# Optimization experiments

Hardware: AMD Instinct MI355X
Metric: run time of the kernel (lower is better)

The kernel has to match this reference:

```python
import jax, jax.numpy as jnp
import numpy as np

DIM = 512
H = 8
HD = DIM // H  # head_dim = 64


def setup_inputs() -> dict:
    key = jax.random.key(0)
    k1, k2, k3 = jax.random.split(key, 3)
    B, N = 16, 4096
    x = jax.random.normal(k1, (B, DIM, N), jnp.float32)
    # qkv_proj: Conv1d(dim, H*(1+2*HD), kernel=1) == linear over channels
    Wqkv = jax.random.normal(k2, (H * (1 + 2 * HD), DIM), jnp.float32) * 0.02
    bqkv = jnp.zeros((H * (1 + 2 * HD),), jnp.float32)
    # proj: Conv1d(dim, dim, kernel=1)
    Wp = jax.random.normal(k3, (DIM, DIM), jnp.float32) * 0.02
    bp = jnp.zeros((DIM,), jnp.float32)
    return {"x": x, "Wqkv": Wqkv, "bqkv": bqkv, "Wp": Wp, "bp": bp}


def reference(x, Wqkv, bqkv, Wp, bp):
    B, C, N = x.shape
    # 1x1 conv projection -> [B, H*(1+2*HD), N]
    qkv = jnp.einsum('oc,bcn->bon', Wqkv, x) + bqkv[None, :, None]
    qkv = qkv.reshape(B, H, 1 + 2 * HD, N)
    q = qkv[:, :, 0:1, :]          # [B,H,1,N]
    k = qkv[:, :, 1:1 + HD, :]     # [B,H,HD,N]
    v = qkv[:, :, 1 + HD:, :]      # [B,H,HD,N]
    scores = jax.nn.softmax(q, axis=-1)              # softmax over N
    ctx = jnp.sum(k * scores, axis=-1, keepdims=True)  # [B,H,HD,1]
    out = jax.nn.relu(v) * ctx                         # [B,H,HD,N]
    # permute/split/cat in torch == [B,H,HD,N] -> [B,N,H*HD] -> [B,C,N]
    out = out.transpose(0, 3, 1, 2).reshape(B, N, H * HD)
    out = out.transpose(0, 2, 1)                       # [B,C,N]
    out = jnp.einsum('oc,bcn->bon', Wp, out) + bp[None, :, None]
    return out
```

## Files before the change

kernel.cpp:

```cpp
#include <hip/hip_runtime.h>

#define NB 16
#define NC 512
#define NN 4096
#define NH 8

typedef __attribute__((ext_vector_type(8))) __bf16 bf16x8;
typedef __attribute__((ext_vector_type(4))) float f32x4;

__device__ __forceinline__ unsigned short f2bf(float f) {
    union { float f; unsigned u; } x; x.f = f;
    unsigned r = x.u + 0x7FFF + ((x.u >> 16) & 1);
    return (unsigned short)(r >> 16);
}
__device__ __forceinline__ float bits2f(unsigned u) {
    union { unsigned u; float f; } x; x.u = u; return x.f;
}

__global__ void pack_kernel(const float* __restrict__ Wqkv, const float* __restrict__ bqkv,
                            const float* __restrict__ Wp,
                            unsigned short* __restrict__ Wv_bf, unsigned short* __restrict__ Wp_bf,
                            float* __restrict__ bv) {
    int t = blockIdx.x * 256 + threadIdx.x;
    int j = t >> 9, c = t & 511;
    int h = j >> 6, d = j & 63;
    Wv_bf[t] = f2bf(Wqkv[((size_t)h * 129 + 65 + d) * 512 + c]);
    Wp_bf[t] = f2bf(Wp[t]);
    if (t < 512) bv[t] = bqkv[(t >> 6) * 129 + 65 + (t & 63)];
}

__global__ void transpose_q_kernel(const float* __restrict__ x, const float* __restrict__ Wqkv,
                                   unsigned short* __restrict__ xT, float* __restrict__ qP) {
    __shared__ unsigned short tile[64][66];
    __shared__ float Ws[8][64];
    __shared__ float qw[4][8][64];
    int b = blockIdx.z, c0 = blockIdx.y * 64, n0 = blockIdx.x * 64;
    int t = threadIdx.x;
    for (int i = t; i < 512; i += 256)
        Ws[i >> 6][i & 63] = Wqkv[(size_t)(i >> 6) * (129 * 512) + c0 + (i & 63)];
    __syncthreads();
    int r = t >> 4, cc = (t & 15) * 4;
    const float* xp = x + ((size_t)b * NC + c0) * NN + n0;
    float accq[8][4];
#pragma unroll
    for (int h = 0; h < 8; h++)
#pragma unroll
        for (int j = 0; j < 4; j++) accq[h][j] = 0.f;
#pragma unroll
    for (int p = 0; p < 4; p++) {
        int row = r + p * 16;
        float4 v = *(const float4*)(xp + (size_t)row * NN + cc);
        tile[row][cc + 0] = f2bf(v.x);
        tile[row][cc + 1] = f2bf(v.y);
        tile[row][cc + 2] = f2bf(v.z);
        tile[row][cc + 3] = f2bf(v.w);
#pragma unroll
        for (int h = 0; h < 8; h++) {
            float w = Ws[h][row];
            accq[h][0] += w * v.x;
            accq[h][1] += w * v.y;
            accq[h][2] += w * v.z;
            accq[h][3] += w * v.w;
        }
    }
    __syncthreads();
    {
        int j = t >> 2, cg = (t & 3) * 16;
        alignas(16) unsigned short tmp[16];
#pragma unroll
        for (int i = 0; i < 16; i++) tmp[i] = tile[cg + i][j];
        unsigned short* dst = xT + ((size_t)b * NN + n0 + j) * NC + c0 + cg;
        *(uint4*)(dst) = *(const uint4*)(tmp);
        *(uint4*)(dst + 8) = *(const uint4*)(tmp + 8);
    }
    int lane = t & 63, w = t >> 6;
#pragma unroll
    for (int h = 0; h < 8; h++)
#pragma unroll
        for (int j = 0; j < 4; j++) {
            float a = accq[h][j];
            a += __shfl_xor(a, 16);
            a += __shfl_xor(a, 32);
            accq[h][j] = a;
        }
    if (lane < 16) {
#pragma unroll
        for (int h = 0; h < 8; h++)
#pragma unroll
            for (int j = 0; j < 4; j++) qw[w][h][lane * 4 + j] = accq[h][j];
    }
    __syncthreads();
    for (int i = t; i < 512; i += 256) {
        int h = i >> 6, n = i & 63;
        float s = qw[0][h][n] + qw[1][h][n] + qw[2][h][n] + qw[3][h][n];
        qP[(((size_t)blockIdx.y * NB + b) * 8 + h) * NN + n0 + n] = s;
    }
}

__global__ void softmax_kernel(const float* __restrict__ qP, float* __restrict__ sT) {
    int bh = blockIdx.x;
    int b = bh >> 3, h = bh & 7;
    int t = threadIdx.x;
    __shared__ float red[8];
    const float* qp = qP + (size_t)bh * NN;
    const size_t cstr = (size_t)NB * 8 * NN;
    float v[16];
    float mx = -1e30f;
#pragma unroll
    for (int i = 0; i < 16; i++) {
        int n = t + i * 256;
        float s = 0.f;
#pragma unroll
        for (int cb = 0; cb < 8; cb++) s += qp[cb * cstr + n];
        v[i] = s; mx = fmaxf(mx, s);
    }
#pragma unroll
    for (int o = 32; o; o >>= 1) mx = fmaxf(mx, __shfl_xor(mx, o));
    if ((t & 63) == 0) red[t >> 6] = mx;
    __syncthreads();
    mx = fmaxf(fmaxf(red[0], red[1]), fmaxf(red[2], red[3]));
    float s = 0.f;
#pragma unroll
    for (int i = 0; i < 16; i++) { v[i] = __expf(v[i] - mx); s += v[i]; }
#pragma unroll
    for (int o = 32; o; o >>= 1) s += __shfl_xor(s, o);
    __syncthreads();
    if ((t & 63) == 0) red[4 + (t >> 6)] = s;
    __syncthreads();
    float inv = 1.f / (red[4] + red[5] + red[6] + red[7]);
#pragma unroll
    for (int i = 0; i < 16; i++) {
        int n = t + i * 256;
        sT[((size_t)b * NN + n) * 8 + h] = v[i] * inv;
    }
}

__global__ void xbar_kernel(const unsigned short* __restrict__ xT, const float* __restrict__ sT,
                            float* __restrict__ xbarP) {
    int b = blockIdx.y, sl = blockIdx.x;
    int t = threadIdx.x;
    int g = __builtin_amdgcn_readfirstlane(t >> 6);
    int lane = t & 63;
    int c8 = lane * 8;
    int nbase = sl * 256 + g * 64;
    float acc[8][8];
#pragma unroll
    for (int h = 0; h < 8; h++)
#pragma unroll
        for (int c = 0; c < 8; c++) acc[h][c] = 0.f;
    const unsigned short* xp = xT + ((size_t)b * NN + nbase) * NC + c8;
    const float* sp = sT + ((size_t)b * NN + nbase) * 8;
    for (int i = 0; i < 64; i++) {
        uint4 xv = *(const uint4*)(xp + (size_t)i * NC);
        float xf[8];
        xf[0] = bits2f(xv.x << 16); xf[1] = bits2f(xv.x & 0xFFFF0000u);
        xf[2] = bits2f(xv.y << 16); xf[3] = bits2f(xv.y & 0xFFFF0000u);
        xf[4] = bits2f(xv.z << 16); xf[5] = bits2f(xv.z & 0xFFFF0000u);
        xf[6] = bits2f(xv.w << 16); xf[7] = bits2f(xv.w & 0xFFFF0000u);
#pragma unroll
        for (int h = 0; h < 8; h++) {
            float s = sp[i * 8 + h];
#pragma unroll
            for (int c = 0; c < 8; c++) acc[h][c] += s * xf[c];
        }
    }
#pragma unroll
    for (int h = 0; h < 8; h++) {
        float* dst = xbarP + (((size_t)(sl * 4 + g) * NB + b) * 8 + h) * NC + c8;
        f32x4 lo = {acc[h][0], acc[h][1], acc[h][2], acc[h][3]};
        f32x4 hi = {acc[h][4], acc[h][5], acc[h][6], acc[h][7]};
        *(f32x4*)(dst) = lo;
        *(f32x4*)(dst + 4) = hi;
    }
}

__global__ void ctx_kernel(const float* __restrict__ xbarP, const float* __restrict__ Wqkv,
                           const float* __restrict__ bqkv, float* __restrict__ ctx) {
    int bh = blockIdx.x; int b = bh >> 3, h = bh & 7;
    int t = threadIdx.x;
    __shared__ float xb[512];
    for (int i = t; i < 512; i += 256) {
        float s = 0.f;
        for (int sl = 0; sl < 64; sl++) s += xbarP[(((size_t)sl * NB + b) * 8 + h) * NC + i];
        xb[i] = s;
    }
    __syncthreads();
    int d = t >> 2, sub = t & 3;
    const float* wk = Wqkv + ((size_t)h * 129 + 1 + d) * 512;
    float acc = 0.f;
    for (int i = sub * 4; i < 512; i += 16) {
        float4 w = *(const float4*)(wk + i);
        acc += w.x * xb[i] + w.y * xb[i + 1] + w.z * xb[i + 2] + w.w * xb[i + 3];
    }
    acc += __shfl_xor(acc, 1);
    acc += __shfl_xor(acc, 2);
    if (sub == 0) ctx[(size_t)b * NC + h * 64 + d] = acc + bqkv[h * 129 + 1 + d];
}

template <int MODE>
__global__ __launch_bounds__(512) void gemm_kernel(
    const unsigned short* __restrict__ A,
    const unsigned short* __restrict__ Bmat,
    const float* __restrict__ bias,
    const float* __restrict__ ctx,
    unsigned short* __restrict__ mT,
    float* __restrict__ outp)
{
    __shared__ alignas(16) unsigned short As[256 * 32];
    __shared__ alignas(16) unsigned short Bs[128 * 32];
    int b = blockIdx.z;
    int m0 = blockIdx.y * 256, n0 = blockIdx.x * 128;
    int t = threadIdx.x;
    int lane = t & 63;
    int wid = t >> 6;
    int wm = wid >> 1, wn = wid & 1;

    const unsigned short* Bb = Bmat + ((size_t)b * NN + n0) * NC;

    f32x4 acc[4][4];
#pragma unroll
    for (int i = 0; i < 4; i++)
#pragma unroll
        for (int j = 0; j < 4; j++) { f32x4 z = {0.f, 0.f, 0.f, 0.f}; acc[i][j] = z; }

    for (int kk = 0; kk < 512; kk += 32) {
        {
            int u = t, row = u >> 2, kg = u & 3;
            uint4 va = *(const uint4*)(A + (size_t)(m0 + row) * 512 + kk + kg * 8);
            *(uint4*)(As + (size_t)u * 8) = va;
            u = t + 512; row = u >> 2; kg = u & 3;
            uint4 vb = *(const uint4*)(A + (size_t)(m0 + row) * 512 + kk + kg * 8);
            *(uint4*)(As + (size_t)u * 8) = vb;
            u = t; row = u >> 2; kg = u & 3;
            uint4 vc = *(const uint4*)(Bb + (size_t)row * 512 + kk + kg * 8);
            *(uint4*)(Bs + (size_t)u * 8) = vc;
        }
        __syncthreads();
        bf16x8 af[4], bfr[4];
        int koff = (lane >> 4) * 8;
        int arow = wm * 64 + (lane & 15);
        int brow = wn * 64 + (lane & 15);
#pragma unroll
        for (int i = 0; i < 4; i++) af[i]  = *(const bf16x8*)(As + (size_t)(arow + i * 16) * 32 + koff);
#pragma unroll
        for (int j = 0; j < 4; j++) bfr[j] = *(const bf16x8*)(Bs + (size_t)(brow + j * 16) * 32 + koff);
#pragma unroll
        for (int i = 0; i < 4; i++)
#pragma unroll
            for (int j = 0; j < 4; j++)
                acc[i][j] = __builtin_amdgcn_mfma_f32_16x16x32_bf16(af[i], bfr[j], acc[i][j], 0, 0, 0);
        __syncthreads();
    }

    int g = lane >> 4, col = lane & 15;
#pragma unroll
    for (int i = 0; i < 4; i++) {
        int j0 = m0 + wm * 64 + i * 16 + g * 4;
        if (MODE == 0) {
            float4 bv4 = *(const float4*)(bias + j0);
            float4 cx4 = *(const float4*)(ctx + (size_t)b * NC + j0);
#pragma unroll
            for (int j = 0; j < 4; j++) {
                int n = n0 + wn * 64 + j * 16 + col;
                f32x4 a = acc[i][j];
                unsigned short h0 = f2bf(fmaxf(a[0] + bv4.x, 0.f) * cx4.x);
                unsigned short h1 = f2bf(fmaxf(a[1] + bv4.y, 0.f) * cx4.y);
                unsigned short h2 = f2bf(fmaxf(a[2] + bv4.z, 0.f) * cx4.z);
                unsigned short h3 = f2bf(fmaxf(a[3] + bv4.w, 0.f) * cx4.w);
                uint2 pk;
                pk.x = (unsigned)h0 | ((unsigned)h1 << 16);
                pk.y = (unsigned)h2 | ((unsigned)h3 << 16);
                *(uint2*)(mT + ((size_t)b * NN + n) * NC + j0) = pk;
            }
        } else {
            float4 bp4 = *(const float4*)(bias + j0);
#pragma unroll
            for (int j = 0; j < 4; j++) {
                int n = n0 + wn * 64 + j * 16 + col;
                f32x4 a = acc[i][j];
                float* op = outp + (size_t)b * NC * NN + (size_t)j0 * NN + n;
                op[0]              = a[0] + bp4.x;
                op[NN]             = a[1] + bp4.y;
                op[2 * (size_t)NN] = a[2] + bp4.z;
                op[3 * (size_t)NN] = a[3] + bp4.w;
            }
        }
    }
}

extern "C" void kernel_launch(void* const* d_in, const int* in_sizes, int n_in,
                              void* d_out, int out_size, void* d_ws, size_t ws_size,
                              hipStream_t stream) {
    const float* x    = (const float*)d_in[0];
    const float* Wqkv = (const float*)d_in[1];
    const float* bqkv = (const float*)d_in[2];
    const float* Wp   = (const float*)d_in[3];
    const float* bp   = (const float*)d_in[4];
    float* outp = (float*)d_out;

    char* ws = (char*)d_ws;
    unsigned short* mT = (unsigned short*)ws;
    float* sT    = (float*)(ws + 2097152);
    float* qP    = (float*)(ws + 4194304);
    float* xbarP = (float*)(ws + 20971520);
    float* ctx   = (float*)(ws + 67108864);
    unsigned short* Wv_bf = (unsigned short*)(ws + 67108864 + 32768);
    unsigned short* Wp_bf = (unsigned short*)(ws + 67108864 + 32768 + 524288);
    float* bv    = (float*)(ws + 67108864 + 32768 + 1048576);
    unsigned short* xT = (unsigned short*)d_out;

    pack_kernel<<<dim3(1024), 256, 0, stream>>>(Wqkv, bqkv, Wp, Wv_bf, Wp_bf, bv);
    transpose_q_kernel<<<dim3(64, 8, 16), 256, 0, stream>>>(x, Wqkv, xT, qP);
    softmax_kernel<<<dim3(128), 256, 0, stream>>>(qP, sT);
    xbar_kernel<<<dim3(16, 16), 256, 0, stream>>>(xT, sT, xbarP);
    ctx_kernel<<<dim3(128), 256, 0, stream>>>(xbarP, Wqkv, bqkv, ctx);
    gemm_kernel<0><<<dim3(32, 2, 16), 512, 0, stream>>>(Wv_bf, xT, bv, ctx, mT, nullptr);
    gemm_kernel<1><<<dim3(32, 2, 16), 512, 0, stream>>>(Wp_bf, mT, bp, nullptr, nullptr, outp);
}
```

Before: 209.1 us.

## Compute full q logits per block over all channels, drop partial-sum buffer

The transpose+q kernel now tiles 32 sequence positions across all 512 channels per block. This lets the q projection be reduced entirely in-block and written once, instead of writing 8 channel-block partials that softmax must re-sum. The softmax kernel reads the final logits directly. In exchange, the block uses much more shared memory and the bf16 transpose is written with 2-byte scalar stores, which may reduce occupancy and store efficiency.

```diff
diff --git a/kernel.cpp b/kernel.cpp
--- a/kernel.cpp
+++ b/kernel.cpp
@@ -29,91 +29,89 @@
     if (t < 512) bv[t] = bqkv[(t >> 6) * 129 + 65 + (t & 63)];
 }
 
-__global__ void transpose_q_kernel(const float* __restrict__ x, const float* __restrict__ Wqkv,
-                                   unsigned short* __restrict__ xT, float* __restrict__ qP) {
-    __shared__ unsigned short tile[64][66];
-    __shared__ float Ws[8][64];
-    __shared__ float qw[4][8][64];
-    int b = blockIdx.z, c0 = blockIdx.y * 64, n0 = blockIdx.x * 64;
-    int t = threadIdx.x;
-    for (int i = t; i < 512; i += 256)
-        Ws[i >> 6][i & 63] = Wqkv[(size_t)(i >> 6) * (129 * 512) + c0 + (i & 63)];
-    __syncthreads();
-    int r = t >> 4, cc = (t & 15) * 4;
-    const float* xp = x + ((size_t)b * NC + c0) * NN + n0;
+__global__ __launch_bounds__(256) void transpose_q_kernel(
+        const float* __restrict__ x, const float* __restrict__ Wqkv,
+        unsigned short* __restrict__ xT, float* __restrict__ q) {
+    __shared__ unsigned int tile[512 * 17];
+    __shared__ float Ws[8][512];
+    __shared__ float qw[4][8][32];
+    int b = blockIdx.y, n0 = blockIdx.x * 32;
+    int t = threadIdx.x;
+
+    for (int i = t; i < 4096; i += 256)
+        Ws[i >> 9][i & 511] = Wqkv[(size_t)(i >> 9) * (129 * 512) + (i & 511)];
+    __syncthreads();
+
+    int k = t & 7;
+    int r0 = t >> 3;
     float accq[8][4];
 #pragma unroll
     for (int h = 0; h < 8; h++)
 #pragma unroll
         for (int j = 0; j < 4; j++) accq[h][j] = 0.f;
-#pragma unroll
-    for (int p = 0; p < 4; p++) {
-        int row = r + p * 16;
-        float4 v = *(const float4*)(xp + (size_t)row * NN + cc);
-        tile[row][cc + 0] = f2bf(v.x);
-        tile[row][cc + 1] = f2bf(v.y);
-        tile[row][cc + 2] = f2bf(v.z);
-        tile[row][cc + 3] = f2bf(v.w);
+    const float* xp = x + (size_t)b * NC * NN + n0 + 4 * k;
+#pragma unroll 4
+    for (int p = 0; p < 16; p++) {
+        int c = r0 + 32 * p;
+        float4 v = *(const float4*)(xp + (size_t)c * NN);
+        unsigned lo = (unsigned)f2bf(v.x) | ((unsigned)f2bf(v.y) << 16);
+        unsigned hi = (unsigned)f2bf(v.z) | ((unsigned)f2bf(v.w) << 16);
+        tile[c * 17 + 2 * k]     = lo;
+        tile[c * 17 + 2 * k + 1] = hi;
 #pragma unroll
         for (int h = 0; h < 8; h++) {
-            float w = Ws[h][row];
+            float w = Ws[h][c];
             accq[h][0] += w * v.x;
             accq[h][1] += w * v.y;
             accq[h][2] += w * v.z;
             accq[h][3] += w * v.w;
         }
     }
-    __syncthreads();
-    {
-        int j = t >> 2, cg = (t & 3) * 16;
-        alignas(16) unsigned short tmp[16];
-#pragma unroll
-        for (int i = 0; i < 16; i++) tmp[i] = tile[cg + i][j];
-        unsigned short* dst = xT + ((size_t)b * NN + n0 + j) * NC + c0 + cg;
-        *(uint4*)(dst) = *(const uint4*)(tmp);
-        *(uint4*)(dst + 8) = *(const uint4*)(tmp + 8);
-    }
-    int lane = t & 63, w = t >> 6;
+    int lane = t & 63, wv = t >> 6;
 #pragma unroll
     for (int h = 0; h < 8; h++)
 #pragma unroll
         for (int j = 0; j < 4; j++) {
             float a = accq[h][j];
+            a += __shfl_xor(a, 8);
             a += __shfl_xor(a, 16);
             a += __shfl_xor(a, 32);
             accq[h][j] = a;
         }
-    if (lane < 16) {
+    if (lane < 8) {
 #pragma unroll
         for (int h = 0; h < 8; h++)
 #pragma unroll
-            for (int j = 0; j < 4; j++) qw[w][h][lane * 4 + j] = accq[h][j];
-    }
-    __syncthreads();
-    for (int i = t; i < 512; i += 256) {
-        int h = i >> 6, n = i & 63;
-        float s = qw[0][h][n] + qw[1][h][n] + qw[2][h][n] + qw[3][h][n];
-        qP[(((size_t)blockIdx.y * NB + b) * 8 + h) * NN + n0 + n] = s;
-    }
-}
-
-__global__ void softmax_kernel(const float* __restrict__ qP, float* __restrict__ sT) {
+            for (int j = 0; j < 4; j++) qw[wv][h][4 * lane + j] = accq[h][j];
+    }
+    __syncthreads();
+    {
+        int h = t >> 5, n = t & 31;
+        q[((size_t)b * 8 + h) * NN + n0 + n] =
+            qw[0][h][n] + qw[1][h][n] + qw[2][h][n] + qw[3][h][n];
+    }
+
+    unsigned short* xb = xT + (size_t)b * NN * NC;
+    for (int it = wv; it < 128; it += 4) {
+        int cw = it >> 4, np = it & 15;
+        int c = cw * 64 + lane;
+        unsigned u = tile[c * 17 + np];
+        int n = n0 + 2 * np;
+        xb[(size_t)n * NC + c]       = (unsigned short)(u & 0xFFFFu);
+        xb[(size_t)(n + 1) * NC + c] = (unsigned short)(u >> 16);
+    }
+}
+
+__global__ void softmax_kernel(const float* __restrict__ q, float* __restrict__ sT) {
     int bh = blockIdx.x;
     int b = bh >> 3, h = bh & 7;
     int t = threadIdx.x;
     __shared__ float red[8];
-    const float* qp = qP + (size_t)bh * NN;
-    const size_t cstr = (size_t)NB * 8 * NN;
+    const float* qp = q + (size_t)bh * NN;
     float v[16];
     float mx = -1e30f;
 #pragma unroll
-    for (int i = 0; i < 16; i++) {
-        int n = t + i * 256;
-        float s = 0.f;
-#pragma unroll
-        for (int cb = 0; cb < 8; cb++) s += qp[cb * cstr + n];
-        v[i] = s; mx = fmaxf(mx, s);
-    }
+    for (int i = 0; i < 16; i++) { v[i] = qp[t + i * 256]; mx = fmaxf(mx, v[i]); }
 #pragma unroll
     for (int o = 32; o; o >>= 1) mx = fmaxf(mx, __shfl_xor(mx, o));
     if ((t & 63) == 0) red[t >> 6] = mx;
@@ -301,7 +299,7 @@
     char* ws = (char*)d_ws;
     unsigned short* mT = (unsigned short*)ws;
     float* sT    = (float*)(ws + 2097152);
-    float* qP    = (float*)(ws + 4194304);
+    float* q     = (float*)(ws + 4194304);
     float* xbarP = (float*)(ws + 20971520);
     float* ctx   = (float*)(ws + 67108864);
     unsigned short* Wv_bf = (unsigned short*)(ws + 67108864 + 32768);
@@ -310,8 +308,8 @@
     unsigned short* xT = (unsigned short*)d_out;
 
     pack_kernel<<<dim3(1024), 256, 0, stream>>>(Wqkv, bqkv, Wp, Wv_bf, Wp_bf, bv);
-    transpose_q_kernel<<<dim3(64, 8, 16), 256, 0, stream>>>(x, Wqkv, xT, qP);
-    softmax_kernel<<<dim3(128), 256, 0, stream>>>(qP, sT);
+    transpose_q_kernel<<<dim3(128, 16), 256, 0, stream>>>(x, Wqkv, xT, q);
+    softmax_kernel<<<dim3(128), 256, 0, stream>>>(q, sT);
     xbar_kernel<<<dim3(16, 16), 256, 0, stream>>>(xT, sT, xbarP);
     ctx_kernel<<<dim3(128), 256, 0, stream>>>(xbarP, Wqkv, bqkv, ctx);
     gemm_kernel<0><<<dim3(32, 2, 16), 512, 0, stream>>>(Wv_bf, xT, bv, ctx, mT, nullptr);
```

New measurement: 215.6 us. 1.03x slower.

## Keep x in channel-major bf16, drop transpose, async LDS loads in GEMM

Applied to the files above, without the earlier changes.

The first pass now writes x converted to bf16 in its original [B,C,N] layout instead of transposing it to [B,N,C]. It still fuses the q projection, which removes the shared-memory transpose. The xbar reduction is restructured around this layout with shuffle and LDS reductions, and the partial-slice count drops from 64 to 8. In the GEMMs, the A operand and the MODE 1 B operand use global_load_lds async copies. MODE 0 scatters the channel-major x into a swizzled LDS tile, which costs uncoalesced 2-byte LDS stores in exchange for avoiding the transpose.

```diff
diff --git a/kernel.cpp b/kernel.cpp
--- a/kernel.cpp
+++ b/kernel.cpp
@@ -15,6 +15,12 @@
 }
 __device__ __forceinline__ float bits2f(unsigned u) {
     union { unsigned u; float f; } x; x.u = u; return x.f;
+}
+
+__device__ __forceinline__ void async16(const void* g, const void* l) {
+    __builtin_amdgcn_global_load_lds(
+        (const __attribute__((address_space(1))) void*)g,
+        (__attribute__((address_space(3))) void*)l, 16, 0, 0);
 }
 
 __global__ void pack_kernel(const float* __restrict__ Wqkv, const float* __restrict__ bqkv,
@@ -29,71 +35,38 @@
     if (t < 512) bv[t] = bqkv[(t >> 6) * 129 + 65 + (t & 63)];
 }
 
-__global__ void transpose_q_kernel(const float* __restrict__ x, const float* __restrict__ Wqkv,
-                                   unsigned short* __restrict__ xT, float* __restrict__ qP) {
-    __shared__ unsigned short tile[64][66];
+__global__ __launch_bounds__(256) void q_xbf_kernel(
+        const float* __restrict__ x, const float* __restrict__ Wqkv,
+        unsigned int* __restrict__ xbf, float* __restrict__ qP) {
     __shared__ float Ws[8][64];
-    __shared__ float qw[4][8][64];
-    int b = blockIdx.z, c0 = blockIdx.y * 64, n0 = blockIdx.x * 64;
+    int n0 = blockIdx.x * 512, c0 = blockIdx.y * 64, b = blockIdx.z;
     int t = threadIdx.x;
     for (int i = t; i < 512; i += 256)
         Ws[i >> 6][i & 63] = Wqkv[(size_t)(i >> 6) * (129 * 512) + c0 + (i & 63)];
     __syncthreads();
-    int r = t >> 4, cc = (t & 15) * 4;
-    const float* xp = x + ((size_t)b * NC + c0) * NN + n0;
-    float accq[8][4];
-#pragma unroll
-    for (int h = 0; h < 8; h++)
-#pragma unroll
-        for (int j = 0; j < 4; j++) accq[h][j] = 0.f;
-#pragma unroll
-    for (int p = 0; p < 4; p++) {
-        int row = r + p * 16;
-        float4 v = *(const float4*)(xp + (size_t)row * NN + cc);
-        tile[row][cc + 0] = f2bf(v.x);
-        tile[row][cc + 1] = f2bf(v.y);
-        tile[row][cc + 2] = f2bf(v.z);
-        tile[row][cc + 3] = f2bf(v.w);
+
+    float acc[8][2];
+#pragma unroll
+    for (int h = 0; h < 8; h++) { acc[h][0] = 0.f; acc[h][1] = 0.f; }
+
+    const float* xb = x + ((size_t)b * NC + c0) * NN + n0;
+    unsigned int* ob = xbf + (((size_t)b * NC + c0) * NN + n0) / 2 + t;
+
+#pragma unroll 4
+    for (int c = 0; c < 64; c++) {
+        float2 v = *((const float2*)(xb + (size_t)c * NN) + t);
+        ob[(size_t)c * (NN / 2)] = (unsigned)f2bf(v.x) | ((unsigned)f2bf(v.y) << 16);
 #pragma unroll
         for (int h = 0; h < 8; h++) {
-            float w = Ws[h][row];
-            accq[h][0] += w * v.x;
-            accq[h][1] += w * v.y;
-            accq[h][2] += w * v.z;
-            accq[h][3] += w * v.w;
-        }
-    }
-    __syncthreads();
-    {
-        int j = t >> 2, cg = (t & 3) * 16;
-        alignas(16) unsigned short tmp[16];
-#pragma unroll
-        for (int i = 0; i < 16; i++) tmp[i] = tile[cg + i][j];
-        unsigned short* dst = xT + ((size_t)b * NN + n0 + j) * NC + c0 + cg;
-        *(uint4*)(dst) = *(const uint4*)(tmp);
-        *(uint4*)(dst + 8) = *(const uint4*)(tmp + 8);
-    }
-    int lane = t & 63, w = t >> 6;
-#pragma unroll
-    for (int h = 0; h < 8; h++)
-#pragma unroll
-        for (int j = 0; j < 4; j++) {
-            float a = accq[h][j];
-            a += __shfl_xor(a, 16);
-            a += __shfl_xor(a, 32);
-            accq[h][j] = a;
-        }
-    if (lane < 16) {
-#pragma unroll
-        for (int h = 0; h < 8; h++)
-#pragma unroll
-            for (int j = 0; j < 4; j++) qw[w][h][lane * 4 + j] = accq[h][j];
-    }
-    __syncthreads();
-    for (int i = t; i < 512; i += 256) {
-        int h = i >> 6, n = i & 63;
-        float s = qw[0][h][n] + qw[1][h][n] + qw[2][h][n] + qw[3][h][n];
-        qP[(((size_t)blockIdx.y * NB + b) * 8 + h) * NN + n0 + n] = s;
+            float w = Ws[h][c];
+            acc[h][0] += w * v.x;
+            acc[h][1] += w * v.y;
+        }
+    }
+#pragma unroll
+    for (int h = 0; h < 8; h++) {
+        float2 o; o.x = acc[h][0]; o.y = acc[h][1];
+        *((float2*)(qP + ((size_t)(blockIdx.y * NB + b) * 8 + h) * NN + n0) + t) = o;
     }
 }
 
@@ -135,42 +108,70 @@
     }
 }
 
-__global__ void xbar_kernel(const unsigned short* __restrict__ xT, const float* __restrict__ sT,
-                            float* __restrict__ xbarP) {
-    int b = blockIdx.y, sl = blockIdx.x;
-    int t = threadIdx.x;
-    int g = __builtin_amdgcn_readfirstlane(t >> 6);
-    int lane = t & 63;
-    int c8 = lane * 8;
-    int nbase = sl * 256 + g * 64;
+__global__ __launch_bounds__(256) void xbar_kernel(
+        const unsigned int* __restrict__ xbf, const float* __restrict__ sT,
+        float* __restrict__ xbarP) {
+    __shared__ float red[4][8][64];
+    int c0 = blockIdx.x * 32, sl = blockIdx.y, b = blockIdx.z;
+    int t = threadIdx.x;
+    int l = t & 63, w = t >> 6;
+    int nsl0 = sl * 512;
+    float s_[8][8];
+    {
+        const f32x4* sp = (const f32x4*)(sT + ((size_t)b * NN + nsl0 + l * 8) * 8);
+#pragma unroll
+        for (int j = 0; j < 8; j++) {
+            f32x4 a = sp[2 * j], bq = sp[2 * j + 1];
+            s_[j][0] = a[0]; s_[j][1] = a[1]; s_[j][2] = a[2]; s_[j][3] = a[3];
+            s_[j][4] = bq[0]; s_[j][5] = bq[1]; s_[j][6] = bq[2]; s_[j][7] = bq[3];
+        }
+    }
     float acc[8][8];
 #pragma unroll
-    for (int h = 0; h < 8; h++)
-#pragma unroll
-        for (int c = 0; c < 8; c++) acc[h][c] = 0.f;
-    const unsigned short* xp = xT + ((size_t)b * NN + nbase) * NC + c8;
-    const float* sp = sT + ((size_t)b * NN + nbase) * 8;
-    for (int i = 0; i < 64; i++) {
-        uint4 xv = *(const uint4*)(xp + (size_t)i * NC);
+    for (int r = 0; r < 8; r++)
+#pragma unroll
+        for (int h = 0; h < 8; h++) acc[r][h] = 0.f;
+
+    const unsigned int* xr = xbf + (((size_t)b * NC + c0 + w * 8) * NN + nsl0) / 2 + l * 4;
+    uint4 xv = *(const uint4*)(xr);
+#pragma unroll
+    for (int r = 0; r < 8; r++) {
+        uint4 cur = xv;
+        if (r < 7) xv = *(const uint4*)(xr + (size_t)(r + 1) * (NN / 2));
         float xf[8];
-        xf[0] = bits2f(xv.x << 16); xf[1] = bits2f(xv.x & 0xFFFF0000u);
-        xf[2] = bits2f(xv.y << 16); xf[3] = bits2f(xv.y & 0xFFFF0000u);
-        xf[4] = bits2f(xv.z << 16); xf[5] = bits2f(xv.z & 0xFFFF0000u);
-        xf[6] = bits2f(xv.w << 16); xf[7] = bits2f(xv.w & 0xFFFF0000u);
+        xf[0] = bits2f(cur.x << 16); xf[1] = bits2f(cur.x & 0xFFFF0000u);
+        xf[2] = bits2f(cur.y << 16); xf[3] = bits2f(cur.y & 0xFFFF0000u);
+        xf[4] = bits2f(cur.z << 16); xf[5] = bits2f(cur.z & 0xFFFF0000u);
+        xf[6] = bits2f(cur.w << 16); xf[7] = bits2f(cur.w & 0xFFFF0000u);
+#pragma unroll
+        for (int j = 0; j < 8; j++)
+#pragma unroll
+            for (int h = 0; h < 8; h++) acc[r][h] += xf[j] * s_[j][h];
+    }
+#pragma unroll
+    for (int r = 0; r < 8; r++)
 #pragma unroll
         for (int h = 0; h < 8; h++) {
-            float s = sp[i * 8 + h];
-#pragma unroll
-            for (int c = 0; c < 8; c++) acc[h][c] += s * xf[c];
-        }
-    }
-#pragma unroll
-    for (int h = 0; h < 8; h++) {
-        float* dst = xbarP + (((size_t)(sl * 4 + g) * NB + b) * 8 + h) * NC + c8;
-        f32x4 lo = {acc[h][0], acc[h][1], acc[h][2], acc[h][3]};
-        f32x4 hi = {acc[h][4], acc[h][5], acc[h][6], acc[h][7]};
-        *(f32x4*)(dst) = lo;
-        *(f32x4*)(dst + 4) = hi;
+            float a = acc[r][h];
+            a += __shfl_xor(a, 8);
+            a += __shfl_xor(a, 16);
+            a += __shfl_xor(a, 32);
+            acc[r][h] = a;
+        }
+    if (l < 8) {
+#pragma unroll
+        for (int r = 0; r < 8; r++)
+#pragma unroll
+            for (int h = 0; h < 8; h++) red[w][l][r * 8 + h] = acc[r][h];
+    }
+    __syncthreads();
+    {
+        int idx = t & 63;
+        float v = 0.f;
+#pragma unroll
+        for (int res = 0; res < 8; res++) v += red[w][res][idx];
+        int r = idx >> 3, h = idx & 7;
+        xbarP[(((size_t)sl * NB + b) * 8 + h) * NC + c0 + w * 8 + r] = v;
     }
 }
 
@@ -181,7 +182,8 @@
     __shared__ float xb[512];
     for (int i = t; i < 512; i += 256) {
         float s = 0.f;
-        for (int sl = 0; sl < 64; sl++) s += xbarP[(((size_t)sl * NB + b) * 8 + h) * NC + i];
+#pragma unroll
+        for (int sl = 0; sl < 8; sl++) s += xbarP[(((size_t)sl * NB + b) * 8 + h) * NC + i];
         xb[i] = s;
     }
     __syncthreads();
@@ -216,6 +218,9 @@
     int wm = wid >> 1, wn = wid & 1;
 
     const unsigned short* Bb = Bmat + ((size_t)b * NN + n0) * NC;
+    const unsigned int*   Bu = (const unsigned int*)Bmat + (size_t)b * NC * (NN / 2);
+
+    int srow = lane >> 2, sc8 = (lane & 3) * 8;
 
     f32x4 acc[4][4];
 #pragma unroll
@@ -224,16 +229,20 @@
         for (int j = 0; j < 4; j++) { f32x4 z = {0.f, 0.f, 0.f, 0.f}; acc[i][j] = z; }
 
     for (int kk = 0; kk < 512; kk += 32) {
-        {
-            int u = t, row = u >> 2, kg = u & 3;
-            uint4 va = *(const uint4*)(A + (size_t)(m0 + row) * 512 + kk + kg * 8);
-            *(uint4*)(As + (size_t)u * 8) = va;
-            u = t + 512; row = u >> 2; kg = u & 3;
-            uint4 vb = *(const uint4*)(A + (size_t)(m0 + row) * 512 + kk + kg * 8);
-            *(uint4*)(As + (size_t)u * 8) = vb;
-            u = t; row = u >> 2; kg = u & 3;
-            uint4 vc = *(const uint4*)(Bb + (size_t)row * 512 + kk + kg * 8);
-            *(uint4*)(Bs + (size_t)u * 8) = vc;
+        async16(A + (size_t)(m0 + wid * 32 + srow) * 512 + kk + sc8,      As + wid * 1024);
+        async16(A + (size_t)(m0 + wid * 32 + 16 + srow) * 512 + kk + sc8, As + wid * 1024 + 512);
+        if constexpr (MODE == 0) {
+            int c = t >> 4, nb = (t & 15) * 8;
+            uint4 xv = *(const uint4*)(Bu + ((size_t)(kk + c) * NN + n0 + nb) / 2);
+            const unsigned short* xp16 = (const unsigned short*)&xv;
+#pragma unroll
+            for (int i = 0; i < 8; i++) {
+                int nl = nb + i;
+                int byte = nl * 64 + ((c * 2) ^ (((nl >> 3) & 3) << 4));
+                *(unsigned short*)((char*)Bs + byte) = xp16[i];
+            }
+        } else {
+            async16(Bb + (size_t)(wid * 16 + srow) * 512 + kk + sc8, Bs + wid * 512);
         }
         __syncthreads();
         bf16x8 af[4], bfr[4];
@@ -243,7 +252,15 @@
 #pragma unroll
         for (int i = 0; i < 4; i++) af[i]  = *(const bf16x8*)(As + (size_t)(arow + i * 16) * 32 + koff);
 #pragma unroll
-        for (int j = 0; j < 4; j++) bfr[j] = *(const bf16x8*)(Bs + (size_t)(brow + j * 16) * 32 + koff);
+        for (int j = 0; j < 4; j++) {
+            if constexpr (MODE == 0) {
+                int row = brow + j * 16;
+                int byte = row * 64 + ((koff * 2) ^ (((row >> 3) & 3) << 4));
+                bfr[j] = *(const bf16x8*)((const char*)Bs + byte);
+            } else {
+                bfr[j] = *(const bf16x8*)(Bs + (size_t)(brow + j * 16) * 32 + koff);
+            }
+        }
 #pragma unroll
         for (int i = 0; i < 4; i++)
 #pragma unroll
@@ -307,13 +324,15 @@
     unsigned short* Wv_bf = (unsigned short*)(ws + 67108864 + 32768);
     unsigned short* Wp_bf = (unsigned short*)(ws + 67108864 + 32768 + 524288);
     float* bv    = (float*)(ws + 67108864 + 32768 + 1048576);
-    unsigned short* xT = (unsigned short*)d_out;
+    unsigned int* xbf = (unsigned int*)d_out;
 
     pack_kernel<<<dim3(1024), 256, 0, stream>>>(Wqkv, bqkv, Wp, Wv_bf, Wp_bf, bv);
-    transpose_q_kernel<<<dim3(64, 8, 16), 256, 0, stream>>>(x, Wqkv, xT, qP);
+    q_xbf_kernel<<<dim3(8, 8, 16), 256, 0, stream>>>(x, Wqkv, xbf, qP);
     softmax_kernel<<<dim3(128), 256, 0, stream>>>(qP, sT);
-    xbar_kernel<<<dim3(16, 16), 256, 0, stream>>>(xT, sT, xbarP);
+    xbar_kernel<<<dim3(16, 8, 16), 256, 0, stream>>>(xbf, sT, xbarP);
     ctx_kernel<<<dim3(128), 256, 0, stream>>>(xbarP, Wqkv, bqkv, ctx);
-    gemm_kernel<0><<<dim3(32, 2, 16), 512, 0, stream>>>(Wv_bf, xT, bv, ctx, mT, nullptr);
-    gemm_kernel<1><<<dim3(32, 2, 16), 512, 0, stream>>>(Wp_bf, mT, bp, nullptr, nullptr, outp);
-}
+    gemm_kernel<0><<<dim3(32, 2, 16), 512, 0, stream>>>(
+        Wv_bf, (const unsigned short*)xbf, bv, ctx, mT, nullptr);
+    gemm_kernel<1><<<dim3(32, 2, 16), 512, 0, stream>>>(
+        Wp_bf, mT, bp, nullptr, nullptr, outp);
+}
```

Result: slower. 219.3 us (+4.9%).
